# Kernel optimization log

Measured on AMD Instinct MI355X. Metric: run time of the kernel, lower is better.

## Reference

```python
import jax, jax.numpy as jnp
import numpy as np
from jax import lax

B, T = 16384, 10
H = 256
CAR_V, REG_V, POI_V, WEEK_V, TIME_V = 1000000, 100000, 1000, 7, 1440
LABELS = 500
IN = 39  # 16+8+4+3+8


def _lstm_layer(x, Wih, Whh, bih, bhh):
    # x: [B, T, D] -> outputs [B, T, H]; PyTorch gate order i,f,g,o
    b = x.shape[0]
    h0 = jnp.zeros((b, H), x.dtype)
    c0 = jnp.zeros((b, H), x.dtype)
    # Precompute input projections for all timesteps in one GEMM
    xg = jnp.einsum('btd,gd->btg', x, Wih) + bih + bhh  # [B, T, 4H]

    def step(carry, xt_g):
        h, c = carry
        gates = xt_g + h @ Whh.T  # [B, 4H]
        i, f, g, o = jnp.split(gates, 4, axis=-1)
        i, f, o = jax.nn.sigmoid(i), jax.nn.sigmoid(f), jax.nn.sigmoid(o)
        g = jnp.tanh(g)
        c = f * c + i * g
        h = o * jnp.tanh(c)
        return (h, c), h

    _, ys = lax.scan(step, (h0, c0), xg.transpose(1, 0, 2))  # ys: [T, B, H]
    return ys.transpose(1, 0, 2)


def setup_inputs() -> dict:
    key = jax.random.key(0)
    ks = jax.random.split(key, 20)
    s = 0.05
    return {
        'car_idx': jax.random.randint(ks[0], (B, T), 0, CAR_V),
        'region_idx': jax.random.randint(ks[1], (B, T), 0, REG_V),
        'poi_idx': jax.random.randint(ks[2], (B, T), 0, POI_V),
        'week_idx': jax.random.randint(ks[3], (B, T), 0, WEEK_V),
        'time_idx': jax.random.randint(ks[4], (B, T), 0, TIME_V),
        'car_emb': jax.random.normal(ks[5], (CAR_V, 16), jnp.float32) * s,
        'region_emb': jax.random.normal(ks[6], (REG_V, 8), jnp.float32) * s,
        'poi_emb': jax.random.normal(ks[7], (POI_V, 4), jnp.float32) * s,
        'week_emb': jax.random.normal(ks[8], (WEEK_V, 3), jnp.float32) * s,
        'time_emb': jax.random.normal(ks[9], (TIME_V, 8), jnp.float32) * s,
        'Wih0': jax.random.normal(ks[10], (4 * H, IN), jnp.float32) * s,
        'Whh0': jax.random.normal(ks[11], (4 * H, H), jnp.float32) * s,
        'bih0': jax.random.normal(ks[12], (4 * H,), jnp.float32) * s,
        'bhh0': jax.random.normal(ks[13], (4 * H,), jnp.float32) * s,
        'Wih1': jax.random.normal(ks[14], (4 * H, H), jnp.float32) * s,
        'Whh1': jax.random.normal(ks[15], (4 * H, H), jnp.float32) * s,
        'bih1': jax.random.normal(ks[16], (4 * H,), jnp.float32) * s,
        'bhh1': jax.random.normal(ks[17], (4 * H,), jnp.float32) * s,
        'Wout': jax.random.normal(ks[18], (LABELS, H), jnp.float32) * s,
        'bout': jax.random.normal(ks[19], (LABELS,), jnp.float32) * s,
    }


def reference(car_idx, region_idx, poi_idx, week_idx, time_idx,
              car_emb, region_emb, poi_emb, week_emb, time_emb,
              Wih0, Whh0, bih0, bhh0, Wih1, Whh1, bih1, bhh1,
              Wout, bout):
    # Batched version of the original per-item embedding-lookup + concat loop
    x = jnp.concatenate([
        car_emb[car_idx],      # [B, T, 16]
        region_emb[region_idx],  # [B, T, 8]
        poi_emb[poi_idx],      # [B, T, 4]
        week_emb[week_idx],    # [B, T, 3]
        time_emb[time_idx],    # [B, T, 8]
    ], axis=-1)  # [B, T, 39]
    h1 = _lstm_layer(x, Wih0, Whh0, bih0, bhh0)
    h2 = _lstm_layer(h1, Wih1, Whh1, bih1, bhh1)
    return h2[:, -1, :] @ Wout.T + bout  # [B, LABELS]
```

## Files before the change

kernel.cpp:

```cpp
#include <hip/hip_runtime.h>
#include <hip/hip_bf16.h>

#define BB 16384
#define TT 10
#define NLAB 500

typedef __attribute__((ext_vector_type(8))) __bf16 bf16x8;
typedef __attribute__((ext_vector_type(4))) float f32x4;
typedef __attribute__((ext_vector_type(8))) short short8v;

__device__ __forceinline__ unsigned short f2bf(float f) {
  union { float f; unsigned int u; } x; x.f = f;
  unsigned int r = 0x7fffu + ((x.u >> 16) & 1u);
  return (unsigned short)((x.u + r) >> 16);
}

__device__ __forceinline__ float sigm(float x) {
  return __builtin_amdgcn_rcpf(1.f + __builtin_amdgcn_exp2f(-1.4426950408889634f * x));
}
__device__ __forceinline__ float tanh_(float x) {
  float e = __builtin_amdgcn_exp2f(-2.8853900817779268f * x);
  return 2.f * __builtin_amdgcn_rcpf(1.f + e) - 1.f;
}

__device__ __forceinline__ void gload_lds16(const unsigned short* g, unsigned short* l) {
  __builtin_amdgcn_global_load_lds(
      (const __attribute__((address_space(1))) unsigned int*)g,
      (__attribute__((address_space(3))) unsigned int*)l, 16, 0, 0);
}

#define SCHED0() __builtin_amdgcn_sched_barrier(0)
#define BAR_LGKM()                                                       \
  { SCHED0(); asm volatile("s_waitcnt lgkmcnt(0)" ::: "memory");         \
    __builtin_amdgcn_s_barrier(); SCHED0(); }
#define BAR_LGKM_VM4()                                                   \
  { SCHED0(); asm volatile("s_waitcnt vmcnt(4) lgkmcnt(0)" ::: "memory");\
    __builtin_amdgcn_s_barrier(); SCHED0(); }

__global__ void prep_w(const float* __restrict__ Wih0, const float* __restrict__ Whh0,
                       const float* __restrict__ bih0, const float* __restrict__ bhh0,
                       const float* __restrict__ Wih1, const float* __restrict__ Whh1,
                       const float* __restrict__ bih1, const float* __restrict__ bhh1,
                       const float* __restrict__ Wout, const float* __restrict__ bout,
                       unsigned short* __restrict__ wall, float* __restrict__ bblob) {
  int i = blockIdx.x * 256 + threadIdx.x;
  if (i < 983040) {
    int c = i >> 14, r = i & 16383;
    int wid = r >> 11, frag = (r >> 9) & 3, lane = (r >> 3) & 63, e = r & 7;
    int kin = ((lane >> 4) << 3) + e;
    float v;
    if (c < 20) {
      int pass = c / 10, ks = c % 10;
      int n = (pass * 2 + (frag >> 1)) * 256 + wid * 32 + (frag & 1) * 16 + (lane & 15);
      int k = ks * 32 + kin;
      if (k < 64) v = (k < 39) ? Wih0[n * 39 + k] : 0.f;
      else        v = Whh0[n * 256 + (k - 64)];
    } else if (c < 52) {
      int idx = c - 20;
      int pass = idx >> 4, half = (idx >> 3) & 1, ks = idx & 7;
      int n = (pass * 2 + (frag >> 1)) * 256 + wid * 32 + (frag & 1) * 16 + (lane & 15);
      int k = ks * 32 + kin;
      v = half ? Wih1[n * 256 + k]
               : Whh1[n * 256 + k];
    } else {
      int ks = c - 52;
      int n = wid * 64 + frag * 16 + (lane & 15);
      int k = ks * 32 + kin;
      v = (n < NLAB) ? Wout[n * 256 + k] : 0.f;
    }
    wall[i] = f2bf(v);
  } else {
    int j = i - 983040;
    if (j < 1024)       bblob[j] = bih0[j] + bhh0[j];
    else if (j < 2048)  bblob[j] = bih1[j - 1024] + bhh1[j - 1024];
    else if (j < 2560) { int n = j - 2048; bblob[j] = (n < NLAB) ? bout[n] : 0.f; }
  }
}

__global__ void gather_x(const int* __restrict__ car_idx, const int* __restrict__ region_idx,
                         const int* __restrict__ poi_idx, const int* __restrict__ week_idx,
                         const int* __restrict__ time_idx,
                         const float* __restrict__ car_emb, const float* __restrict__ region_emb,
                         const float* __restrict__ poi_emb, const float* __restrict__ week_emb,
                         const float* __restrict__ time_emb,
                         unsigned short* __restrict__ xfrag) {
  int tid = blockIdx.x * 256 + threadIdx.x;
  if (tid >= BB * TT) return;
  int t = tid / BB;
  int b = tid - t * BB;
  int ii = b * TT + t;
  float v[64];
#pragma unroll
  for (int k = 0; k < 64; ++k) v[k] = 0.f;
  { const float* p = car_emb + (size_t)car_idx[ii] * 16;
#pragma unroll
    for (int k = 0; k < 16; ++k) v[k] = p[k]; }
  { const float* p = region_emb + (size_t)region_idx[ii] * 8;
#pragma unroll
    for (int k = 0; k < 8; ++k) v[16 + k] = p[k]; }
  { const float* p = poi_emb + (size_t)poi_idx[ii] * 4;
#pragma unroll
    for (int k = 0; k < 4; ++k) v[24 + k] = p[k]; }
  { const float* p = week_emb + (size_t)week_idx[ii] * 3;
#pragma unroll
    for (int k = 0; k < 3; ++k) v[28 + k] = p[k]; }
  { const float* p = time_emb + (size_t)time_idx[ii] * 8;
#pragma unroll
    for (int k = 0; k < 8; ++k) v[31 + k] = p[k]; }

  int tile = b >> 6, rb = (b >> 4) & 3, lrow = b & 15;
  size_t base = ((size_t)tile * TT + t) * 4096;
#pragma unroll
  for (int c = 0; c < 8; ++c) {
    int kc = c >> 2;
    int lane = lrow + ((c & 3) << 4);
    size_t off = base + (size_t)((((kc << 2) + rb) << 6) + lane) * 8;
    short8v s;
#pragma unroll
    for (int e = 0; e < 8; ++e) s[e] = (short)f2bf(v[c * 8 + e]);
    *(short8v*)(xfrag + off) = s;
  }
}

__device__ __forceinline__ f32x4 MF(bf16x8 a, bf16x8 b, f32x4 c) {
  return __builtin_amdgcn_mfma_f32_16x16x32_bf16(a, b, c, 0, 0, 0);
}

template <int NKS, int SPLIT>
__device__ __forceinline__ void gemm_pass(f32x4 (&acc)[2][2][4], bf16x8 (&bc)[4],
    const unsigned short* wp, const unsigned short* wnext,
    const unsigned short* ab1, const unsigned short* ab2, int lane) {
#define AADDR(KS) \
  ((SPLIT < NKS && (KS) >= SPLIT) ? (ab2 + ((KS) - SPLIT) * 2048) : (ab1 + (KS) * 2048))
  bf16x8 aA[4], aB[4];
  {
    const unsigned short* a0 = AADDR(0);
#pragma unroll
    for (int rb = 0; rb < 4; ++rb) aA[rb] = *(const bf16x8*)(a0 + rb * 512 + lane * 8);
  }
#pragma unroll 1
  for (int ks = 0; ks < NKS; ks += 2) {
    bf16x8 bn[4];
    const unsigned short* w1 = wp + 16384;
#pragma unroll
    for (int f = 0; f < 4; ++f) bn[f] = *(const bf16x8*)(w1 + f * 512);
    const unsigned short* an = AADDR(ks + 1);
#pragma unroll
    for (int rb = 0; rb < 4; ++rb) aB[rb] = *(const bf16x8*)(an + rb * 512 + lane * 8);
    __builtin_amdgcn_s_setprio(1);
#pragma unroll
    for (int gl = 0; gl < 2; ++gl)
#pragma unroll
      for (int nb = 0; nb < 2; ++nb)
#pragma unroll
        for (int rb = 0; rb < 4; ++rb)
          acc[gl][nb][rb] = MF(aA[rb], bc[gl * 2 + nb], acc[gl][nb][rb]);
    __builtin_amdgcn_s_setprio(0);
    const unsigned short* w2 = (ks + 2 < NKS) ? (wp + 32768) : wnext;
#pragma unroll
    for (int f = 0; f < 4; ++f) bc[f] = *(const bf16x8*)(w2 + f * 512);
    const unsigned short* an2 = AADDR((ks + 2 < NKS) ? (ks + 2) : (NKS - 1));
#pragma unroll
    for (int rb = 0; rb < 4; ++rb) aA[rb] = *(const bf16x8*)(an2 + rb * 512 + lane * 8);
    __builtin_amdgcn_s_setprio(1);
#pragma unroll
    for (int gl = 0; gl < 2; ++gl)
#pragma unroll
      for (int nb = 0; nb < 2; ++nb)
#pragma unroll
        for (int rb = 0; rb < 4; ++rb)
          acc[gl][nb][rb] = MF(aB[rb], bn[gl * 2 + nb], acc[gl][nb][rb]);
    __builtin_amdgcn_s_setprio(0);
    wp += 32768;
  }
#undef AADDR
}

__device__ __forceinline__ void partial_if(f32x4 (&acc)[2][2][4], f32x4 (&cst)[2][4],
                                           float* sib) {
#pragma unroll
  for (int nb = 0; nb < 2; ++nb)
#pragma unroll
    for (int rb = 0; rb < 4; ++rb)
#pragma unroll
      for (int r = 0; r < 4; ++r) {
        sib[((nb << 4) + (rb << 2) + r) << 6] = sigm(acc[0][nb][rb][r]);
        cst[nb][rb][r] = sigm(acc[1][nb][rb][r]) * cst[nb][rb][r];
      }
}

__device__ __forceinline__ void finish_go(f32x4 (&acc)[2][2][4], f32x4 (&cst)[2][4],
    const float* sib, unsigned short* hbuf, int lane, int wid) {
  int lrow = ((lane >> 4) << 2);
  int l15 = lane & 15;
#pragma unroll
  for (int nb = 0; nb < 2; ++nb) {
    int jw = (nb << 4) + l15;
    int lane_dst_base = ((jw >> 3) << 4);
    int elem = jw & 7;
#pragma unroll
    for (int rb = 0; rb < 4; ++rb)
#pragma unroll
      for (int r = 0; r < 4; ++r) {
        float g = tanh_(acc[0][nb][rb][r]);
        float o = sigm(acc[1][nb][rb][r]);
        float c = cst[nb][rb][r] + sib[((nb << 4) + (rb << 2) + r) << 6] * g;
        cst[nb][rb][r] = c;
        float h = o * tanh_(c);
        int lane_dst = lrow + r + lane_dst_base;
        hbuf[(size_t)((((wid << 2) + rb) << 6) + lane_dst) * 8 + elem] = f2bf(h);
      }
  }
}

__global__ __launch_bounds__(512, 1) void lstm_fused(
    const unsigned short* __restrict__ xfrag, const unsigned short* __restrict__ wall,
    const float* __restrict__ bblob, float* __restrict__ out) {
  __shared__ __align__(16) unsigned short h1s[16384];
  __shared__ __align__(16) unsigned short h2s[16384];
  __shared__ __align__(16) unsigned short xts[4096];
  __shared__ __align__(16) float bls[2560];
  __shared__ __align__(16) float sis[16384];

  int tid = threadIdx.x, lane = tid & 63, wid = tid >> 6;
  int tile = blockIdx.x, b0 = tile << 6, l15 = lane & 15;

  for (int i = tid; i < 2560; i += 512) bls[i] = bblob[i];
  gload_lds16(xfrag + (size_t)(tile * TT) * 4096 + wid * 512 + lane * 8, xts + wid * 512);

  float* sib = sis + (wid << 11) + lane;

  const unsigned short* wb = wall + wid * 2048 + lane * 8;

  bf16x8 bc[4];
#pragma unroll
  for (int f = 0; f < 4; ++f) bc[f] = *(const bf16x8*)(wb + f * 512);

  asm volatile("s_waitcnt vmcnt(0)" ::: "memory");
  __syncthreads();

  f32x4 c1[2][4], c2[2][4];
#pragma unroll
  for (int nb = 0; nb < 2; ++nb)
#pragma unroll
    for (int rb = 0; rb < 4; ++rb) {
      c1[nb][rb] = (f32x4){0.f, 0.f, 0.f, 0.f};
      c2[nb][rb] = (f32x4){0.f, 0.f, 0.f, 0.f};
    }
  f32x4 acc[2][2][4];

#define ACC_BIAS(BOFF, GBASE)                                                     \
  _Pragma("unroll")                                                               \
  for (int gl = 0; gl < 2; ++gl)                                                  \
    _Pragma("unroll")                                                             \
    for (int nb = 0; nb < 2; ++nb) {                                              \
      float bv = bls[(BOFF) + (((GBASE) + gl) << 8) + (wid << 5) + (nb << 4) + l15]; \
      _Pragma("unroll")                                                           \
      for (int rb = 0; rb < 4; ++rb) acc[gl][nb][rb] = (f32x4){bv, bv, bv, bv};   \
    }

  ACC_BIAS(0, 0)
  gemm_pass<2, 2>(acc, bc, wb, wb + 163840, xts, xts, lane);
  partial_if(acc, c1, sib);
  ACC_BIAS(0, 2)
  gemm_pass<2, 2>(acc, bc, wb + 163840, wb + 458752, xts, xts, lane);
  BAR_LGKM()
  gload_lds16(xfrag + (size_t)(tile * TT + 1) * 4096 + wid * 512 + lane * 8,
              xts + wid * 512);
  finish_go(acc, c1, sib, h1s, lane, wid);
  ACC_BIAS(1024, 0)
  BAR_LGKM()
  gemm_pass<8, 8>(acc, bc, wb + 458752, wb + 720896, h1s, h1s, lane);
  partial_if(acc, c2, sib);
  ACC_BIAS(1024, 2)
  gemm_pass<8, 8>(acc, bc, wb + 720896, wb, h1s, h1s, lane);
  BAR_LGKM_VM4()
  finish_go(acc, c2, sib, h2s, lane, wid);

#pragma unroll 1
  for (int t = 1; t < TT; ++t) {
    ACC_BIAS(0, 0)
    gemm_pass<10, 2>(acc, bc, wb, wb + 163840, xts, h1s, lane);
    partial_if(acc, c1, sib);
    ACC_BIAS(0, 2)
    gemm_pass<10, 2>(acc, bc, wb + 163840, wb + 327680, xts, h1s, lane);
    BAR_LGKM()
    if (t < TT - 1)
      gload_lds16(xfrag + (size_t)(tile * TT + t + 1) * 4096 + wid * 512 + lane * 8,
                  xts + wid * 512);
    finish_go(acc, c1, sib, h1s, lane, wid);
    ACC_BIAS(1024, 0)
    gemm_pass<8, 8>(acc, bc, wb + 327680, wb + 458752, h2s, h2s, lane);
    BAR_LGKM()
    gemm_pass<8, 8>(acc, bc, wb + 458752, wb + 589824, h1s, h1s, lane);
    partial_if(acc, c2, sib);
    ACC_BIAS(1024, 2)
    gemm_pass<16, 8>(acc, bc, wb + 589824,
                     (t < TT - 1) ? wb : (wb + 851968), h2s, h1s, lane);
    BAR_LGKM_VM4()
    finish_go(acc, c2, sib, h2s, lane, wid);
  }
  BAR_LGKM()

#pragma unroll
  for (int gl = 0; gl < 2; ++gl)
#pragma unroll
    for (int nb = 0; nb < 2; ++nb) {
      float bv = bls[2048 + (wid << 6) + ((gl * 2 + nb) << 4) + l15];
#pragma unroll
      for (int rb = 0; rb < 4; ++rb) acc[gl][nb][rb] = (f32x4){bv, bv, bv, bv};
    }
  gemm_pass<8, 8>(acc, bc, wb + 851968, wb + 851968, h2s, h2s, lane);

#pragma unroll
  for (int gl = 0; gl < 2; ++gl)
#pragma unroll
    for (int nb = 0; nb < 2; ++nb) {
      int n = (wid << 6) + ((gl * 2 + nb) << 4) + l15;
      if (n < NLAB) {
#pragma unroll
        for (int rb = 0; rb < 4; ++rb)
#pragma unroll
          for (int r = 0; r < 4; ++r) {
            int row = (rb << 4) + ((lane >> 4) << 2) + r;
            out[(size_t)(b0 + row) * NLAB + n] = acc[gl][nb][rb][r];
          }
      }
    }
#undef ACC_BIAS
}

extern "C" void kernel_launch(void* const* d_in, const int* in_sizes, int n_in,
                              void* d_out, int out_size, void* d_ws, size_t ws_size,
                              hipStream_t stream) {
  const int* car_idx    = (const int*)d_in[0];
  const int* region_idx = (const int*)d_in[1];
  const int* poi_idx    = (const int*)d_in[2];
  const int* week_idx   = (const int*)d_in[3];
  const int* time_idx   = (const int*)d_in[4];
  const float* car_emb    = (const float*)d_in[5];
  const float* region_emb = (const float*)d_in[6];
  const float* poi_emb    = (const float*)d_in[7];
  const float* week_emb   = (const float*)d_in[8];
  const float* time_emb   = (const float*)d_in[9];
  const float* Wih0 = (const float*)d_in[10];
  const float* Whh0 = (const float*)d_in[11];
  const float* bih0 = (const float*)d_in[12];
  const float* bhh0 = (const float*)d_in[13];
  const float* Wih1 = (const float*)d_in[14];
  const float* Whh1 = (const float*)d_in[15];
  const float* bih1 = (const float*)d_in[16];
  const float* bhh1 = (const float*)d_in[17];
  const float* Wout = (const float*)d_in[18];
  const float* bout = (const float*)d_in[19];

  unsigned short* xfrag = (unsigned short*)d_ws;
  unsigned short* wallp = xfrag + 10485760;
  float* bblob = (float*)(wallp + 983040);

  prep_w<<<3850, 256, 0, stream>>>(Wih0, Whh0, bih0, bhh0, Wih1, Whh1, bih1, bhh1,
                                   Wout, bout, wallp, bblob);
  gather_x<<<640, 256, 0, stream>>>(car_idx, region_idx, poi_idx, week_idx, time_idx,
                                    car_emb, region_emb, poi_emb, week_emb, time_emb, xfrag);
  lstm_fused<<<256, 512, 0, stream>>>(xfrag, wallp, bblob, (float*)d_out);
}
```

Before: 269.6 us.

## Switch LSTM GEMMs from 16x16x32 to 32x32x16 bf16 MFMA tiles

Replaces the 16x16x32 MFMA with the 32x32x16 variant throughout the fused LSTM kernel. The weight pre-packing, input fragment layout, hidden-state write-back and output epilogue are all re-laid-out to match the 32x32 operand and accumulator fragments. This halves the MFMA instruction count per K-step and raises the operand reuse of each loaded fragment, at the cost of a different accumulator register layout and more complex scatter indexing in the gate epilogue.

Result: slower. 304.5 us (+13.0%).

```diff
diff --git a/kernel.cpp b/kernel.cpp
--- a/kernel.cpp
+++ b/kernel.cpp
@@ -6,7 +6,7 @@
 #define NLAB 500
 
 typedef __attribute__((ext_vector_type(8))) __bf16 bf16x8;
-typedef __attribute__((ext_vector_type(4))) float f32x4;
+typedef __attribute__((ext_vector_type(16))) float f32x16;
 typedef __attribute__((ext_vector_type(8))) short short8v;
 
 __device__ __forceinline__ unsigned short f2bf(float f) {
@@ -46,25 +46,26 @@
   int i = blockIdx.x * 256 + threadIdx.x;
   if (i < 983040) {
     int c = i >> 14, r = i & 16383;
-    int wid = r >> 11, frag = (r >> 9) & 3, lane = (r >> 3) & 63, e = r & 7;
-    int kin = ((lane >> 4) << 3) + e;
+    int wid = r >> 11, gl = (r >> 10) & 1, kh = (r >> 9) & 1, lane = (r >> 3) & 63, e = r & 7;
+    int col = lane & 31;
+    int kin = kh * 16 + ((lane >> 5) << 3) + e;
     float v;
     if (c < 20) {
       int pass = c / 10, ks = c % 10;
-      int n = (pass * 2 + (frag >> 1)) * 256 + wid * 32 + (frag & 1) * 16 + (lane & 15);
+      int n = (pass * 2 + gl) * 256 + wid * 32 + col;
       int k = ks * 32 + kin;
       if (k < 64) v = (k < 39) ? Wih0[n * 39 + k] : 0.f;
       else        v = Whh0[n * 256 + (k - 64)];
     } else if (c < 52) {
       int idx = c - 20;
       int pass = idx >> 4, half = (idx >> 3) & 1, ks = idx & 7;
-      int n = (pass * 2 + (frag >> 1)) * 256 + wid * 32 + (frag & 1) * 16 + (lane & 15);
+      int n = (pass * 2 + gl) * 256 + wid * 32 + col;
       int k = ks * 32 + kin;
       v = half ? Wih1[n * 256 + k]
                : Whh1[n * 256 + k];
     } else {
       int ks = c - 52;
-      int n = wid * 64 + frag * 16 + (lane & 15);
+      int n = wid * 64 + gl * 32 + col;
       int k = ks * 32 + kin;
       v = (n < NLAB) ? Wout[n * 256 + k] : 0.f;
     }
@@ -108,13 +109,13 @@
 #pragma unroll
     for (int k = 0; k < 8; ++k) v[31 + k] = p[k]; }
 
-  int tile = b >> 6, rb = (b >> 4) & 3, lrow = b & 15;
+  int tile = b >> 6, rb = (b >> 5) & 1, lrow = b & 31;
   size_t base = ((size_t)tile * TT + t) * 4096;
 #pragma unroll
   for (int c = 0; c < 8; ++c) {
-    int kc = c >> 2;
-    int lane = lrow + ((c & 3) << 4);
-    size_t off = base + (size_t)((((kc << 2) + rb) << 6) + lane) * 8;
+    int kc = c >> 2, kh = (c >> 1) & 1, kb = c & 1;
+    int lane = lrow + (kb << 5);
+    size_t off = base + (size_t)((((((kc << 1) + kh) << 1) + rb) << 6) + lane) * 8;
     short8v s;
 #pragma unroll
     for (int e = 0; e < 8; ++e) s[e] = (short)f2bf(v[c * 8 + e]);
@@ -122,21 +123,32 @@
   }
 }
 
-__device__ __forceinline__ f32x4 MF(bf16x8 a, bf16x8 b, f32x4 c) {
-  return __builtin_amdgcn_mfma_f32_16x16x32_bf16(a, b, c, 0, 0, 0);
+__device__ __forceinline__ f32x16 MF32(bf16x8 a, bf16x8 b, f32x16 c) {
+  return __builtin_amdgcn_mfma_f32_32x32x16_bf16(a, b, c, 0, 0, 0);
 }
 
 template <int NKS, int SPLIT>
-__device__ __forceinline__ void gemm_pass(f32x4 (&acc)[2][2][4], bf16x8 (&bc)[4],
+__device__ __forceinline__ void gemm_pass(f32x16 (&acc)[2][2], bf16x8 (&bc)[4],
     const unsigned short* wp, const unsigned short* wnext,
     const unsigned short* ab1, const unsigned short* ab2, int lane) {
 #define AADDR(KS) \
   ((SPLIT < NKS && (KS) >= SPLIT) ? (ab2 + ((KS) - SPLIT) * 2048) : (ab1 + (KS) * 2048))
+#define MFMA8(AR, BR)                                                   \
+  { __builtin_amdgcn_s_setprio(1);                                     \
+    _Pragma("unroll")                                                   \
+    for (int kh = 0; kh < 2; ++kh)                                      \
+      _Pragma("unroll")                                                 \
+      for (int gl = 0; gl < 2; ++gl)                                    \
+        _Pragma("unroll")                                               \
+        for (int rb = 0; rb < 2; ++rb)                                  \
+          acc[gl][rb] = MF32(AR[kh * 2 + rb], BR[gl * 2 + kh], acc[gl][rb]); \
+    __builtin_amdgcn_s_setprio(0); }
+
   bf16x8 aA[4], aB[4];
   {
-    const unsigned short* a0 = AADDR(0);
-#pragma unroll
-    for (int rb = 0; rb < 4; ++rb) aA[rb] = *(const bf16x8*)(a0 + rb * 512 + lane * 8);
+    const unsigned short* ap = AADDR(0);
+#pragma unroll
+    for (int f = 0; f < 4; ++f) aA[f] = *(const bf16x8*)(ap + f * 512 + lane * 8);
   }
 #pragma unroll 1
   for (int ks = 0; ks < NKS; ks += 2) {
@@ -146,71 +158,52 @@
     for (int f = 0; f < 4; ++f) bn[f] = *(const bf16x8*)(w1 + f * 512);
     const unsigned short* an = AADDR(ks + 1);
 #pragma unroll
-    for (int rb = 0; rb < 4; ++rb) aB[rb] = *(const bf16x8*)(an + rb * 512 + lane * 8);
-    __builtin_amdgcn_s_setprio(1);
-#pragma unroll
-    for (int gl = 0; gl < 2; ++gl)
-#pragma unroll
-      for (int nb = 0; nb < 2; ++nb)
-#pragma unroll
-        for (int rb = 0; rb < 4; ++rb)
-          acc[gl][nb][rb] = MF(aA[rb], bc[gl * 2 + nb], acc[gl][nb][rb]);
-    __builtin_amdgcn_s_setprio(0);
+    for (int f = 0; f < 4; ++f) aB[f] = *(const bf16x8*)(an + f * 512 + lane * 8);
+    MFMA8(aA, bc)
     const unsigned short* w2 = (ks + 2 < NKS) ? (wp + 32768) : wnext;
 #pragma unroll
     for (int f = 0; f < 4; ++f) bc[f] = *(const bf16x8*)(w2 + f * 512);
     const unsigned short* an2 = AADDR((ks + 2 < NKS) ? (ks + 2) : (NKS - 1));
 #pragma unroll
-    for (int rb = 0; rb < 4; ++rb) aA[rb] = *(const bf16x8*)(an2 + rb * 512 + lane * 8);
-    __builtin_amdgcn_s_setprio(1);
-#pragma unroll
-    for (int gl = 0; gl < 2; ++gl)
-#pragma unroll
-      for (int nb = 0; nb < 2; ++nb)
-#pragma unroll
-        for (int rb = 0; rb < 4; ++rb)
-          acc[gl][nb][rb] = MF(aB[rb], bn[gl * 2 + nb], acc[gl][nb][rb]);
-    __builtin_amdgcn_s_setprio(0);
+    for (int f = 0; f < 4; ++f) aA[f] = *(const bf16x8*)(an2 + f * 512 + lane * 8);
+    MFMA8(aB, bn)
     wp += 32768;
   }
+#undef MFMA8
 #undef AADDR
 }
 
-__device__ __forceinline__ void partial_if(f32x4 (&acc)[2][2][4], f32x4 (&cst)[2][4],
+__device__ __forceinline__ void partial_if(f32x16 (&acc)[2][2], f32x16 (&cst)[2],
                                            float* sib) {
 #pragma unroll
-  for (int nb = 0; nb < 2; ++nb)
-#pragma unroll
-    for (int rb = 0; rb < 4; ++rb)
-#pragma unroll
-      for (int r = 0; r < 4; ++r) {
-        sib[((nb << 4) + (rb << 2) + r) << 6] = sigm(acc[0][nb][rb][r]);
-        cst[nb][rb][r] = sigm(acc[1][nb][rb][r]) * cst[nb][rb][r];
-      }
-}
-
-__device__ __forceinline__ void finish_go(f32x4 (&acc)[2][2][4], f32x4 (&cst)[2][4],
+  for (int rb = 0; rb < 2; ++rb)
+#pragma unroll
+    for (int r = 0; r < 16; ++r) {
+      sib[((rb << 4) + r) << 6] = sigm(acc[0][rb][r]);
+      cst[rb][r] = sigm(acc[1][rb][r]) * cst[rb][r];
+    }
+}
+
+__device__ __forceinline__ void finish_go(f32x16 (&acc)[2][2], f32x16 (&cst)[2],
     const float* sib, unsigned short* hbuf, int lane, int wid) {
-  int lrow = ((lane >> 4) << 2);
-  int l15 = lane & 15;
-#pragma unroll
-  for (int nb = 0; nb < 2; ++nb) {
-    int jw = (nb << 4) + l15;
-    int lane_dst_base = ((jw >> 3) << 4);
-    int elem = jw & 7;
-#pragma unroll
-    for (int rb = 0; rb < 4; ++rb)
-#pragma unroll
-      for (int r = 0; r < 4; ++r) {
-        float g = tanh_(acc[0][nb][rb][r]);
-        float o = sigm(acc[1][nb][rb][r]);
-        float c = cst[nb][rb][r] + sib[((nb << 4) + (rb << 2) + r) << 6] * g;
-        cst[nb][rb][r] = c;
-        float h = o * tanh_(c);
-        int lane_dst = lrow + r + lane_dst_base;
-        hbuf[(size_t)((((wid << 2) + rb) << 6) + lane_dst) * 8 + elem] = f2bf(h);
-      }
-  }
+  int e = lane & 7;
+  int kh = (lane >> 4) & 1;
+  int khl = (lane >> 3) & 1;
+  int rbase = (lane >> 5) << 2;
+  unsigned short* base = hbuf + (wid << 11);
+#pragma unroll
+  for (int rb = 0; rb < 2; ++rb)
+#pragma unroll
+    for (int r = 0; r < 16; ++r) {
+      float g = tanh_(acc[0][rb][r]);
+      float o = sigm(acc[1][rb][r]);
+      float c = cst[rb][r] + sib[((rb << 4) + r) << 6] * g;
+      cst[rb][r] = c;
+      float h = o * tanh_(c);
+      int row31 = (r & 3) + ((r >> 2) << 3) + rbase;
+      int lane_dst = row31 + (khl << 5);
+      base[(((kh << 1) + rb) << 9) + (lane_dst << 3) + e] = f2bf(h);
+    }
 }
 
 __global__ __launch_bounds__(512, 1) void lstm_fused(
@@ -223,7 +216,8 @@
   __shared__ __align__(16) float sis[16384];
 
   int tid = threadIdx.x, lane = tid & 63, wid = tid >> 6;
-  int tile = blockIdx.x, b0 = tile << 6, l15 = lane & 15;
+  int tile = blockIdx.x, b0 = tile << 6;
+  int l31 = lane & 31;
 
   for (int i = tid; i < 2560; i += 512) bls[i] = bblob[i];
   gload_lds16(xfrag + (size_t)(tile * TT) * 4096 + wid * 512 + lane * 8, xts + wid * 512);
@@ -239,25 +233,22 @@
   asm volatile("s_waitcnt vmcnt(0)" ::: "memory");
   __syncthreads();
 
-  f32x4 c1[2][4], c2[2][4];
-#pragma unroll
-  for (int nb = 0; nb < 2; ++nb)
-#pragma unroll
-    for (int rb = 0; rb < 4; ++rb) {
-      c1[nb][rb] = (f32x4){0.f, 0.f, 0.f, 0.f};
-      c2[nb][rb] = (f32x4){0.f, 0.f, 0.f, 0.f};
-    }
-  f32x4 acc[2][2][4];
+  f32x16 c1[2], c2[2];
+#pragma unroll
+  for (int rb = 0; rb < 2; ++rb)
+#pragma unroll
+    for (int r = 0; r < 16; ++r) { c1[rb][r] = 0.f; c2[rb][r] = 0.f; }
+  f32x16 acc[2][2];
 
 #define ACC_BIAS(BOFF, GBASE)                                                     \
   _Pragma("unroll")                                                               \
-  for (int gl = 0; gl < 2; ++gl)                                                  \
+  for (int gl = 0; gl < 2; ++gl) {                                                \
+    float bv = bls[(BOFF) + (((GBASE) + gl) << 8) + (wid << 5) + l31];            \
     _Pragma("unroll")                                                             \
-    for (int nb = 0; nb < 2; ++nb) {                                              \
-      float bv = bls[(BOFF) + (((GBASE) + gl) << 8) + (wid << 5) + (nb << 4) + l15]; \
+    for (int rb = 0; rb < 2; ++rb)                                                \
       _Pragma("unroll")                                                           \
-      for (int rb = 0; rb < 4; ++rb) acc[gl][nb][rb] = (f32x4){bv, bv, bv, bv};   \
-    }
+      for (int r = 0; r < 16; ++r) acc[gl][rb][r] = bv;                           \
+  }
 
   ACC_BIAS(0, 0)
   gemm_pass<2, 2>(acc, bc, wb, wb + 163840, xts, xts, lane);
@@ -303,30 +294,31 @@
   BAR_LGKM()
 
 #pragma unroll
-  for (int gl = 0; gl < 2; ++gl)
-#pragma unroll
-    for (int nb = 0; nb < 2; ++nb) {
-      float bv = bls[2048 + (wid << 6) + ((gl * 2 + nb) << 4) + l15];
-#pragma unroll
-      for (int rb = 0; rb < 4; ++rb) acc[gl][nb][rb] = (f32x4){bv, bv, bv, bv};
-    }
+  for (int co = 0; co < 2; ++co) {
+    float bv = bls[2048 + (wid << 6) + (co << 5) + l31];
+#pragma unroll
+    for (int rb = 0; rb < 2; ++rb)
+#pragma unroll
+      for (int r = 0; r < 16; ++r) acc[co][rb][r] = bv;
+  }
   gemm_pass<8, 8>(acc, bc, wb + 851968, wb + 851968, h2s, h2s, lane);
 
-#pragma unroll
-  for (int gl = 0; gl < 2; ++gl)
-#pragma unroll
-    for (int nb = 0; nb < 2; ++nb) {
-      int n = (wid << 6) + ((gl * 2 + nb) << 4) + l15;
+  {
+    int rbase = (lane >> 5) << 2;
+#pragma unroll
+    for (int co = 0; co < 2; ++co) {
+      int n = (wid << 6) + (co << 5) + l31;
       if (n < NLAB) {
 #pragma unroll
-        for (int rb = 0; rb < 4; ++rb)
-#pragma unroll
-          for (int r = 0; r < 4; ++r) {
-            int row = (rb << 4) + ((lane >> 4) << 2) + r;
-            out[(size_t)(b0 + row) * NLAB + n] = acc[gl][nb][rb][r];
+        for (int rb = 0; rb < 2; ++rb)
+#pragma unroll
+          for (int r = 0; r < 16; ++r) {
+            int row = (r & 3) + ((r >> 2) << 3) + rbase + (rb << 5);
+            out[(size_t)(b0 + row) * NLAB + n] = acc[co][rb][r];
           }
       }
     }
+  }
 #undef ACC_BIAS
 }
 
```
